# Kernel tuning notes

Measured on AMD Instinct MI355X. Metric: run time of the kernel, lower is better.

## Reference

```python
import jax, jax.numpy as jnp
import numpy as np

DELAY_TAPS = np.array([1, 4, 24, 96, 168])
MAX_DELAY = int(DELAY_TAPS.max())
LEAK_RATE = 0.1
RESERVOIR_DIM = 256
INPUT_DIM = 1
N_TAPS = len(DELAY_TAPS)
TARGET_RADIUS = 0.95


def setup_inputs() -> dict:
    key = jax.random.key(0)
    kx, kin, kfb, kb = jax.random.split(key, 4)
    B, T = 64, 2048
    x = jax.random.normal(kx, (B, T, INPUT_DIM), dtype=jnp.float32)
    # W_in ~ U(-0.5, 0.5)
    W_in = jax.random.uniform(kin, (RESERVOIR_DIM, INPUT_DIM), dtype=jnp.float32,
                              minval=-0.5, maxval=0.5)
    # W_fb: sparse gaussian rescaled to ~per-tap spectral radius
    per_tap_radius = TARGET_RADIUS / np.sqrt(N_TAPS)
    kfb1, kfb2 = jax.random.split(kfb)
    W = jax.random.normal(kfb1, (N_TAPS, RESERVOIR_DIM, RESERVOIR_DIM), dtype=jnp.float32)
    mask = jax.random.uniform(kfb2, W.shape) < 0.1
    W = W * mask
    # approx spectral radius of sparse gaussian ~ sqrt(R * density)
    approx_radius = np.sqrt(RESERVOIR_DIM * 0.1)
    W_fb = W * (per_tap_radius / approx_radius)
    tap_weights = jnp.ones((N_TAPS,), dtype=jnp.float32)
    bias = jax.random.uniform(kb, (RESERVOIR_DIM,), dtype=jnp.float32,
                              minval=-0.1, maxval=0.1)
    return {"x": x, "W_in": W_in, "W_fb": W_fb,
            "tap_weights": tap_weights, "bias": bias}


def reference(x, W_in, W_fb, tap_weights, bias):
    B, T, _ = x.shape
    R = W_in.shape[0]
    # static gather positions into rolling history buffer of length MAX_DELAY
    # history[:, -1] holds state at t-1  ->  state at t - tau lives at MAX_DELAY - tau
    pos = MAX_DELAY - DELAY_TAPS  # numpy, static

    drive = jnp.einsum('bti,ri->btr', x, W_in)  # (B,T,R)
    tap_w = jax.nn.softmax(tap_weights)

    h0 = jnp.zeros((B, R), x.dtype)
    hist0 = jnp.zeros((B, MAX_DELAY, R), x.dtype)

    def step(carry, d_t):
        h, hist = carry
        delayed = hist[:, pos, :]  # (B,K,R)
        fb = jnp.einsum('k,bkr,krs->bs', tap_w, delayed, W_fb)
        h_new = (1.0 - LEAK_RATE) * h + LEAK_RATE * jnp.tanh(d_t + fb + bias)
        hist = jnp.concatenate([hist[:, 1:], h_new[:, None, :]], axis=1)
        return (h_new, hist), h_new

    drive_t = jnp.swapaxes(drive, 0, 1)  # (T,B,R)
    _, states = jax.lax.scan(step, (h0, hist0), drive_t)
    return jnp.swapaxes(states, 0, 1)  # (B,T,R)
```

## Files before the change

### kernel.cpp

```cpp
#include <hip/hip_runtime.h>
#include <math.h>

typedef __attribute__((ext_vector_type(8))) short bf16x8;
typedef __attribute__((ext_vector_type(4))) float f32x4;

#define BB 64
#define TT 2048
#define RR 256
#define BLK 24
#define NTHR 512
#define HB_PAD 776
#define HW_PAD 264

#define MFMA(a, b, c) __builtin_amdgcn_mfma_f32_16x16x32_bf16((a), (b), (c), 0, 0, 0)

__device__ __forceinline__ unsigned short f2bf(float f) {
    unsigned u = __float_as_uint(f);
    return (unsigned short)((u + 0x7FFFu + ((u >> 16) & 1u)) >> 16);
}
__device__ __forceinline__ float bf2f(unsigned short h) {
    return __uint_as_float(((unsigned)h) << 16);
}
__device__ __forceinline__ float fast_tanh(float x) {
    float e = __expf(2.0f * x);
    return 1.0f - 2.0f * __builtin_amdgcn_rcpf(1.0f + e);
}

__global__ void pack_weights(const float* __restrict__ W_fb,
                             const float* __restrict__ tapw,
                             unsigned short* __restrict__ bp) {
    int gid = blockIdx.x * 256 + threadIdx.x;
    int l = gid & 63, c = gid >> 6;
    int tap = c >> 7;
    int rem = c & 127;
    int kt = rem >> 4, nt = rem & 15;

    float v0 = tapw[0], v1 = tapw[1], v2 = tapw[2], v3 = tapw[3], v4 = tapw[4];
    float mx = fmaxf(fmaxf(fmaxf(v0, v1), fmaxf(v2, v3)), v4);
    float e0 = expf(v0 - mx), e1 = expf(v1 - mx), e2 = expf(v2 - mx),
          e3 = expf(v3 - mx), e4 = expf(v4 - mx);
    float inv = 1.0f / (e0 + e1 + e2 + e3 + e4);
    float tws[5] = {e0 * inv, e1 * inv, e2 * inv, e3 * inv, e4 * inv};
    float tw = tws[tap];

    int kbase = 32 * kt + 8 * (l >> 4);
    int n = 16 * nt + (l & 15);
    const float* W = W_fb + tap * 65536;
    unsigned short t[8];
#pragma unroll
    for (int j = 0; j < 8; ++j) t[j] = f2bf(tw * W[(kbase + j) * 256 + n]);
    uint4 o;
    o.x = (unsigned)t[0] | ((unsigned)t[1] << 16);
    o.y = (unsigned)t[2] | ((unsigned)t[3] << 16);
    o.z = (unsigned)t[4] | ((unsigned)t[5] << 16);
    o.w = (unsigned)t[6] | ((unsigned)t[7] << 16);
    *(uint4*)(bp + (size_t)(c * 64 + l) * 8) = o;
}

__global__ __launch_bounds__(NTHR, 1)
void reservoir_mfma(const float* __restrict__ x,
                    const float* __restrict__ W_in,
                    const float* __restrict__ bias,
                    const unsigned short* __restrict__ bp,
                    float* __restrict__ out)
{
    const int b    = blockIdx.x;
    const int tid  = threadIdx.x;
    const int lane = tid & 63;
    const int w    = tid >> 6;
    const int l15  = lane & 15;
    const int quad = lane >> 4;

    __shared__ float xs[TT];
    __shared__ unsigned short hwinb[8][2][HW_PAD];
    __shared__ unsigned short hbcb[BLK][2][HB_PAD];
    __shared__ float Gl[BLK][257];
    __shared__ float hob[BLK][RR];

    for (int i = tid; i < TT; i += NTHR) xs[i] = x[b * TT + i];
    {
        unsigned* hz = (unsigned*)&hwinb[0][0][0];
        for (int i = tid; i < 8 * 2 * HW_PAD / 2; i += NTHR) hz[i] = 0u;
    }

    const bf16x8* bpv = (const bf16x8*)bp;
    bf16x8 b1[8][2], b4[8][2];
#pragma unroll
    for (int kt = 0; kt < 8; ++kt)
#pragma unroll
        for (int u = 0; u < 2; ++u) {
            int nt = 2 * w + u;
            b1[kt][u] = bpv[((0 * 8 + kt) * 16 + nt) * 64 + lane];
            b4[kt][u] = bpv[((1 * 8 + kt) * 16 + nt) * 64 + lane];
        }

    const int s0g = 32 * w + l15, s1g = s0g + 16;
    const float win0 = W_in[s0g], win1 = W_in[s1g];
    const float bi0 = bias[s0g], bi1 = bias[s1g];
    float hp0 = 0.0f, hp1 = 0.0f;

    const float* outr = out + (size_t)b * TT * RR;
    float*       outw = out + (size_t)b * TT * RR;

    const unsigned short* hw1v = &hwinb[0][l15 & 1][0];
    const unsigned short* hw4v = &hwinb[0][(l15 >> 2) & 1][0];
    const unsigned short* fa1 = &hbcb[16 + (l15 & 7)][(l15 >> 3) & 1][0];
    const size_t HWSLOT = 2 * HW_PAD;

    __syncthreads();

    for (int t0 = 0; t0 < TT; t0 += BLK) {
#pragma unroll
        for (int it = 0; it < 9; ++it) {
            int i = it * NTHR + tid;
            int j = i / 192;
            int p = i - j * 192;
            int r = 4 * p;
            int kf = r >> 8, rr = r & 255;
            float4 v = {0.f, 0.f, 0.f, 0.f};
            if (kf == 0) {
                if (t0 > 0) v = *(const float4*)&hob[j][rr];
            } else {
                int dk = (kf == 1) ? 96 : 168;
                int tt = t0 + j - dk;
                if (tt >= 0) v = *(const float4*)(outr + (size_t)tt * RR + rr);
            }
            unsigned short h0 = f2bf(v.x), h1 = f2bf(v.y), h2 = f2bf(v.z), h3 = f2bf(v.w);
            unsigned short q0 = f2bf(v.x - bf2f(h0)), q1 = f2bf(v.y - bf2f(h1)),
                           q2 = f2bf(v.z - bf2f(h2)), q3 = f2bf(v.w - bf2f(h3));
            uint2 H = { (unsigned)h0 | ((unsigned)h1 << 16), (unsigned)h2 | ((unsigned)h3 << 16) };
            uint2 Q = { (unsigned)q0 | ((unsigned)q1 << 16), (unsigned)q2 | ((unsigned)q3 << 16) };
            *(uint2*)&hbcb[j][0][r] = H;
            *(uint2*)&hbcb[j][1][r] = Q;
        }
        __syncthreads();

        f32x4 zf = {0.f, 0.f, 0.f, 0.f};
        f32x4 cf00a = zf, cf01a = zf, cf00b = zf, cf01b = zf, cf10 = zf, cf11 = zf;
        const int r0a = l15;
        bf16x8 nB0 = bpv[((16 + 0) * 16 + 2 * w + 0) * 64 + lane];
        bf16x8 nB1 = bpv[((16 + 0) * 16 + 2 * w + 1) * 64 + lane];
#pragma unroll 1
        for (int ft = 0; ft < 24; ++ft) {
            bf16x8 B0 = nB0, B1 = nB1;
            int nf = (ft < 23) ? ft + 1 : 23;
            nB0 = bpv[((16 + nf) * 16 + 2 * w + 0) * 64 + lane];
            nB1 = bpv[((16 + nf) * 16 + 2 * w + 1) * 64 + lane];
            int ro = 32 * ft + 8 * quad;
            bf16x8 a00 = *(const bf16x8*)&hbcb[r0a][0][ro];
            bf16x8 a01 = *(const bf16x8*)&hbcb[r0a][1][ro];
            bf16x8 a1  = *(const bf16x8*)&fa1[ro];
            cf00a = MFMA(a00, B0, cf00a); cf01a = MFMA(a00, B1, cf01a);
            cf00b = MFMA(a01, B0, cf00b); cf01b = MFMA(a01, B1, cf01b);
            cf10  = MFMA(a1,  B0, cf10);  cf11  = MFMA(a1,  B1, cf11);
        }
        f32x4 cf00 = cf00a + cf00b, cf01 = cf01a + cf01b;
        float cf10f[4], cf11f[4];
#pragma unroll
        for (int i = 0; i < 4; ++i) {
            cf10f[i] = cf10[i] + __shfl_xor(cf10[i], 32, 64);
            cf11f[i] = cf11[i] + __shfl_xor(cf11[i], 32, 64);
        }
#pragma unroll
        for (int i = 0; i < 4; ++i) {
            int j0 = 4 * quad + i;
            int tx0 = t0 + j0; float xv0 = xs[tx0 < TT ? tx0 : TT - 1];
            Gl[j0][s0g] = cf00[i] + bi0 + xv0 * win0;
            Gl[j0][s1g] = cf01[i] + bi1 + xv0 * win1;
            int j1 = 16 + 4 * quad + i;
            if (j1 < BLK) {
                int tx1 = t0 + j1; float xv1 = xs[tx1 < TT ? tx1 : TT - 1];
                Gl[j1][s0g] = cf10f[i] + bi0 + xv1 * win0;
                Gl[j1][s1g] = cf11f[i] + bi1 + xv1 * win1;
            }
        }
        __syncthreads();

        const int tend = (t0 + BLK < TT) ? (t0 + BLK) : TT;
#pragma unroll 1
        for (int t4 = t0; t4 < tend; t4 += 4) {
            f32x4 c40 = zf, c41 = zf;
            const int sl = (t4 - 4 + (l15 & 3)) & 7;
            const unsigned short* hw4 = hw4v + (size_t)sl * HWSLOT;
#pragma unroll
            for (int kt = 0; kt < 8; ++kt) {
                int ro = 32 * kt + 8 * quad;
                bf16x8 a = *(const bf16x8*)&hw4[ro];
                c40 = MFMA(a, b4[kt][0], c40);
                c41 = MFMA(a, b4[kt][1], c41);
            }
            float c40f[4], c41f[4];
#pragma unroll
            for (int u2 = 0; u2 < 4; ++u2) {
                c40f[u2] = c40[u2] + __shfl_xor(c40[u2], 16, 64);
                c41f[u2] = c41[u2] + __shfl_xor(c41[u2], 16, 64);
            }
#pragma unroll
            for (int u = 0; u < 4; ++u) {
                const int t = t4 + u;
                const int sp = (t - 1) & 7;
                const unsigned short* hw1 = hw1v + (size_t)sp * HWSLOT;
                f32x4 c10 = zf, c11 = zf;
#pragma unroll
                for (int kt = 0; kt < 8; ++kt) {
                    int ro = 32 * kt + 8 * quad;
                    bf16x8 a = *(const bf16x8*)&hw1[ro];
                    c10 = MFMA(a, b1[kt][0], c10);
                    c11 = MFMA(a, b1[kt][1], c11);
                }
                int jj = t - t0;
                float f0 = (c10[0] + c10[1]) + c40f[u] + Gl[jj][s0g];
                float f1 = (c11[0] + c11[1]) + c41f[u] + Gl[jj][s1g];
                float h0 = 0.9f * hp0 + 0.1f * fast_tanh(f0);
                float h1 = 0.9f * hp1 + 0.1f * fast_tanh(f1);
                hp0 = h0; hp1 = h1;
                const int wsl = t & 7;
                if (lane < 16) {
                    unsigned short hh0 = f2bf(h0), hh1 = f2bf(h1);
                    hwinb[wsl][0][s0g] = hh0;
                    hwinb[wsl][0][s1g] = hh1;
                    hwinb[wsl][1][s0g] = f2bf(h0 - bf2f(hh0));
                    hwinb[wsl][1][s1g] = f2bf(h1 - bf2f(hh1));
                    hob[jj][s0g] = h0;
                    hob[jj][s1g] = h1;
                }
                __syncthreads();
            }
        }

        {
            const int nf4 = (tend - t0) * (RR / 4);
            const float4* src = (const float4*)&hob[0][0];
            float4* dst = (float4*)(outw + (size_t)t0 * RR);
#pragma unroll
            for (int it = 0; it < 3; ++it) {
                int idx = it * NTHR + tid;
                if (idx < nf4) dst[idx] = src[idx];
            }
        }
    }
}

extern "C" void kernel_launch(void* const* d_in, const int* in_sizes, int n_in,
                              void* d_out, int out_size, void* d_ws, size_t ws_size,
                              hipStream_t stream) {
    const float* x    = (const float*)d_in[0];
    const float* W_in = (const float*)d_in[1];
    const float* W_fb = (const float*)d_in[2];
    const float* tapw = (const float*)d_in[3];
    const float* bias = (const float*)d_in[4];
    float* out = (float*)d_out;
    unsigned short* bp = (unsigned short*)d_ws;

    pack_weights<<<160, 256, 0, stream>>>(W_fb, tapw, bp);
    reservoir_mfma<<<BB, NTHR, 0, stream>>>(x, W_in, bias, bp, out);
}
```

Before: 2.214 ms.

## Halve block to 4 waves, each owning four 16-column output tiles

```diff
diff --git a/kernel.cpp b/kernel.cpp
--- a/kernel.cpp
+++ b/kernel.cpp
@@ -8,9 +8,9 @@
 #define TT 2048
 #define RR 256
 #define BLK 24
-#define NTHR 512
+#define NTHR 256
 #define HB_PAD 776
-#define HW_PAD 264
+#define HW_PAD 288
 
 #define MFMA(a, b, c) __builtin_amdgcn_mfma_f32_16x16x32_bf16((a), (b), (c), 0, 0, 0)
 
@@ -84,34 +84,38 @@
     }
 
     const bf16x8* bpv = (const bf16x8*)bp;
-    bf16x8 b1[8][2], b4[8][2];
+    bf16x8 b1[8][4], b4[8][4];
 #pragma unroll
     for (int kt = 0; kt < 8; ++kt)
 #pragma unroll
-        for (int u = 0; u < 2; ++u) {
-            int nt = 2 * w + u;
+        for (int u = 0; u < 4; ++u) {
+            int nt = 4 * w + u;
             b1[kt][u] = bpv[((0 * 8 + kt) * 16 + nt) * 64 + lane];
             b4[kt][u] = bpv[((1 * 8 + kt) * 16 + nt) * 64 + lane];
         }
 
-    const int s0g = 32 * w + l15, s1g = s0g + 16;
-    const float win0 = W_in[s0g], win1 = W_in[s1g];
-    const float bi0 = bias[s0g], bi1 = bias[s1g];
-    float hp0 = 0.0f, hp1 = 0.0f;
+    float win[4], bi[4], hp[4];
+#pragma unroll
+    for (int nt = 0; nt < 4; ++nt) {
+        int s = 64 * w + 16 * nt + l15;
+        win[nt] = W_in[s];
+        bi[nt]  = bias[s];
+        hp[nt]  = 0.0f;
+    }
 
     const float* outr = out + (size_t)b * TT * RR;
     float*       outw = out + (size_t)b * TT * RR;
 
     const unsigned short* hw1v = &hwinb[0][l15 & 1][0];
     const unsigned short* hw4v = &hwinb[0][(l15 >> 2) & 1][0];
-    const unsigned short* fa1 = &hbcb[16 + (l15 & 7)][(l15 >> 3) & 1][0];
+    const unsigned short* fa1  = &hbcb[16 + (l15 & 7)][(l15 >> 3) & 1][0];
     const size_t HWSLOT = 2 * HW_PAD;
 
     __syncthreads();
 
     for (int t0 = 0; t0 < TT; t0 += BLK) {
 #pragma unroll
-        for (int it = 0; it < 9; ++it) {
+        for (int it = 0; it < 18; ++it) {
             int i = it * NTHR + tid;
             int j = i / 192;
             int p = i - j * 192;
@@ -136,42 +140,57 @@
         __syncthreads();
 
         f32x4 zf = {0.f, 0.f, 0.f, 0.f};
-        f32x4 cf00a = zf, cf01a = zf, cf00b = zf, cf01b = zf, cf10 = zf, cf11 = zf;
+        f32x4 cf0a[4], cf0b[4], cf1[4];
+#pragma unroll
+        for (int nt = 0; nt < 4; ++nt) { cf0a[nt] = zf; cf0b[nt] = zf; cf1[nt] = zf; }
         const int r0a = l15;
-        bf16x8 nB0 = bpv[((16 + 0) * 16 + 2 * w + 0) * 64 + lane];
-        bf16x8 nB1 = bpv[((16 + 0) * 16 + 2 * w + 1) * 64 + lane];
+        bf16x8 nB[4];
+#pragma unroll
+        for (int nt = 0; nt < 4; ++nt)
+            nB[nt] = bpv[((16 + 0) * 16 + 4 * w + nt) * 64 + lane];
 #pragma unroll 1
         for (int ft = 0; ft < 24; ++ft) {
-            bf16x8 B0 = nB0, B1 = nB1;
+            bf16x8 B[4];
+#pragma unroll
+            for (int nt = 0; nt < 4; ++nt) B[nt] = nB[nt];
             int nf = (ft < 23) ? ft + 1 : 23;
-            nB0 = bpv[((16 + nf) * 16 + 2 * w + 0) * 64 + lane];
-            nB1 = bpv[((16 + nf) * 16 + 2 * w + 1) * 64 + lane];
+#pragma unroll
+            for (int nt = 0; nt < 4; ++nt)
+                nB[nt] = bpv[((16 + nf) * 16 + 4 * w + nt) * 64 + lane];
             int ro = 32 * ft + 8 * quad;
             bf16x8 a00 = *(const bf16x8*)&hbcb[r0a][0][ro];
             bf16x8 a01 = *(const bf16x8*)&hbcb[r0a][1][ro];
             bf16x8 a1  = *(const bf16x8*)&fa1[ro];
-            cf00a = MFMA(a00, B0, cf00a); cf01a = MFMA(a00, B1, cf01a);
-            cf00b = MFMA(a01, B0, cf00b); cf01b = MFMA(a01, B1, cf01b);
-            cf10  = MFMA(a1,  B0, cf10);  cf11  = MFMA(a1,  B1, cf11);
-        }
-        f32x4 cf00 = cf00a + cf00b, cf01 = cf01a + cf01b;
-        float cf10f[4], cf11f[4];
-#pragma unroll
-        for (int i = 0; i < 4; ++i) {
-            cf10f[i] = cf10[i] + __shfl_xor(cf10[i], 32, 64);
-            cf11f[i] = cf11[i] + __shfl_xor(cf11[i], 32, 64);
-        }
+#pragma unroll
+            for (int nt = 0; nt < 4; ++nt) {
+                cf0a[nt] = MFMA(a00, B[nt], cf0a[nt]);
+                cf0b[nt] = MFMA(a01, B[nt], cf0b[nt]);
+                cf1[nt]  = MFMA(a1,  B[nt], cf1[nt]);
+            }
+        }
+        float cf1f[4][4];
+#pragma unroll
+        for (int nt = 0; nt < 4; ++nt)
+#pragma unroll
+            for (int i = 0; i < 4; ++i)
+                cf1f[nt][i] = cf1[nt][i] + __shfl_xor(cf1[nt][i], 32, 64);
 #pragma unroll
         for (int i = 0; i < 4; ++i) {
             int j0 = 4 * quad + i;
             int tx0 = t0 + j0; float xv0 = xs[tx0 < TT ? tx0 : TT - 1];
-            Gl[j0][s0g] = cf00[i] + bi0 + xv0 * win0;
-            Gl[j0][s1g] = cf01[i] + bi1 + xv0 * win1;
+#pragma unroll
+            for (int nt = 0; nt < 4; ++nt) {
+                int s = 64 * w + 16 * nt + l15;
+                Gl[j0][s] = (cf0a[nt][i] + cf0b[nt][i]) + bi[nt] + xv0 * win[nt];
+            }
             int j1 = 16 + 4 * quad + i;
             if (j1 < BLK) {
                 int tx1 = t0 + j1; float xv1 = xs[tx1 < TT ? tx1 : TT - 1];
-                Gl[j1][s0g] = cf10f[i] + bi0 + xv1 * win0;
-                Gl[j1][s1g] = cf11f[i] + bi1 + xv1 * win1;
+#pragma unroll
+                for (int nt = 0; nt < 4; ++nt) {
+                    int s = 64 * w + 16 * nt + l15;
+                    Gl[j1][s] = cf1f[nt][i] + bi[nt] + xv1 * win[nt];
+                }
             }
         }
         __syncthreads();
@@ -179,50 +198,58 @@
         const int tend = (t0 + BLK < TT) ? (t0 + BLK) : TT;
 #pragma unroll 1
         for (int t4 = t0; t4 < tend; t4 += 4) {
-            f32x4 c40 = zf, c41 = zf;
+            f32x4 c4[4];
+#pragma unroll
+            for (int nt = 0; nt < 4; ++nt) c4[nt] = zf;
             const int sl = (t4 - 4 + (l15 & 3)) & 7;
             const unsigned short* hw4 = hw4v + (size_t)sl * HWSLOT;
 #pragma unroll
             for (int kt = 0; kt < 8; ++kt) {
                 int ro = 32 * kt + 8 * quad;
                 bf16x8 a = *(const bf16x8*)&hw4[ro];
-                c40 = MFMA(a, b4[kt][0], c40);
-                c41 = MFMA(a, b4[kt][1], c41);
-            }
-            float c40f[4], c41f[4];
-#pragma unroll
-            for (int u2 = 0; u2 < 4; ++u2) {
-                c40f[u2] = c40[u2] + __shfl_xor(c40[u2], 16, 64);
-                c41f[u2] = c41[u2] + __shfl_xor(c41[u2], 16, 64);
-            }
+#pragma unroll
+                for (int nt = 0; nt < 4; ++nt) c4[nt] = MFMA(a, b4[kt][nt], c4[nt]);
+            }
+            float c4f[4][4];
+#pragma unroll
+            for (int nt = 0; nt < 4; ++nt)
+#pragma unroll
+                for (int u2 = 0; u2 < 4; ++u2)
+                    c4f[nt][u2] = c4[nt][u2] + __shfl_xor(c4[nt][u2], 16, 64);
 #pragma unroll
             for (int u = 0; u < 4; ++u) {
                 const int t = t4 + u;
                 const int sp = (t - 1) & 7;
                 const unsigned short* hw1 = hw1v + (size_t)sp * HWSLOT;
-                f32x4 c10 = zf, c11 = zf;
+                f32x4 c1[4];
+#pragma unroll
+                for (int nt = 0; nt < 4; ++nt) c1[nt] = zf;
 #pragma unroll
                 for (int kt = 0; kt < 8; ++kt) {
                     int ro = 32 * kt + 8 * quad;
                     bf16x8 a = *(const bf16x8*)&hw1[ro];
-                    c10 = MFMA(a, b1[kt][0], c10);
-                    c11 = MFMA(a, b1[kt][1], c11);
-                }
-                int jj = t - t0;
-                float f0 = (c10[0] + c10[1]) + c40f[u] + Gl[jj][s0g];
-                float f1 = (c11[0] + c11[1]) + c41f[u] + Gl[jj][s1g];
-                float h0 = 0.9f * hp0 + 0.1f * fast_tanh(f0);
-                float h1 = 0.9f * hp1 + 0.1f * fast_tanh(f1);
-                hp0 = h0; hp1 = h1;
+#pragma unroll
+                    for (int nt = 0; nt < 4; ++nt) c1[nt] = MFMA(a, b1[kt][nt], c1[nt]);
+                }
+                const int jj = t - t0;
                 const int wsl = t & 7;
+                float hn[4];
+#pragma unroll
+                for (int nt = 0; nt < 4; ++nt) {
+                    int s = 64 * w + 16 * nt + l15;
+                    float f = (c1[nt][0] + c1[nt][1]) + c4f[nt][u] + Gl[jj][s];
+                    hn[nt] = 0.9f * hp[nt] + 0.1f * fast_tanh(f);
+                    hp[nt] = hn[nt];
+                }
                 if (lane < 16) {
-                    unsigned short hh0 = f2bf(h0), hh1 = f2bf(h1);
-                    hwinb[wsl][0][s0g] = hh0;
-                    hwinb[wsl][0][s1g] = hh1;
-                    hwinb[wsl][1][s0g] = f2bf(h0 - bf2f(hh0));
-                    hwinb[wsl][1][s1g] = f2bf(h1 - bf2f(hh1));
-                    hob[jj][s0g] = h0;
-                    hob[jj][s1g] = h1;
+#pragma unroll
+                    for (int nt = 0; nt < 4; ++nt) {
+                        int s = 64 * w + 16 * nt + l15;
+                        unsigned short hh = f2bf(hn[nt]);
+                        hwinb[wsl][0][s] = hh;
+                        hwinb[wsl][1][s] = f2bf(hn[nt] - bf2f(hh));
+                        hob[jj][s] = hn[nt];
+                    }
                 }
                 __syncthreads();
             }
@@ -233,7 +260,7 @@
             const float4* src = (const float4*)&hob[0][0];
             float4* dst = (float4*)(outw + (size_t)t0 * RR);
 #pragma unroll
-            for (int it = 0; it < 3; ++it) {
+            for (int it = 0; it < 6; ++it) {
                 int idx = it * NTHR + tid;
                 if (idx < nf4) dst[idx] = src[idx];
             }
```

Measured after the change: 2.990 ms. 35.1% more time.

## Spread per-step state writes across lanes, pack G as float2, deepen weight prefetch

Applied to the files above, without the earlier changes.

```diff
diff --git a/kernel.cpp b/kernel.cpp
--- a/kernel.cpp
+++ b/kernel.cpp
@@ -10,7 +10,7 @@
 #define BLK 24
 #define NTHR 512
 #define HB_PAD 776
-#define HW_PAD 264
+#define HW_PAD 288
 
 #define MFMA(a, b, c) __builtin_amdgcn_mfma_f32_16x16x32_bf16((a), (b), (c), 0, 0, 0)
 
@@ -74,7 +74,7 @@
     __shared__ float xs[TT];
     __shared__ unsigned short hwinb[8][2][HW_PAD];
     __shared__ unsigned short hbcb[BLK][2][HB_PAD];
-    __shared__ float Gl[BLK][257];
+    __shared__ float2 Gl2[BLK][130];
     __shared__ float hob[BLK][RR];
 
     for (int i = tid; i < TT; i += NTHR) xs[i] = x[b * TT + i];
@@ -104,8 +104,13 @@
 
     const unsigned short* hw1v = &hwinb[0][l15 & 1][0];
     const unsigned short* hw4v = &hwinb[0][(l15 >> 2) & 1][0];
-    const unsigned short* fa1 = &hbcb[16 + (l15 & 7)][(l15 >> 3) & 1][0];
+    const unsigned short* fa1  = &hbcb[16 + (l15 & 7)][(l15 >> 3) & 1][0];
     const size_t HWSLOT = 2 * HW_PAD;
+
+    const int varw  = quad >> 1;
+    const int s_w   = 32 * w + l15 + ((quad & 1) << 4);
+    unsigned short* const hwb = &hwinb[0][0][0];
+    const unsigned hw_off = (unsigned)(varw * HW_PAD + s_w);
 
     __syncthreads();
 
@@ -138,21 +143,52 @@
         f32x4 zf = {0.f, 0.f, 0.f, 0.f};
         f32x4 cf00a = zf, cf01a = zf, cf00b = zf, cf01b = zf, cf10 = zf, cf11 = zf;
         const int r0a = l15;
-        bf16x8 nB0 = bpv[((16 + 0) * 16 + 2 * w + 0) * 64 + lane];
-        bf16x8 nB1 = bpv[((16 + 0) * 16 + 2 * w + 1) * 64 + lane];
+        const int cw0 = 2 * w, cw1 = 2 * w + 1;
+        bf16x8 p0A = bpv[((16 + 0) * 16 + cw0) * 64 + lane];
+        bf16x8 p0B = bpv[((16 + 0) * 16 + cw1) * 64 + lane];
+        bf16x8 p1A = bpv[((16 + 1) * 16 + cw0) * 64 + lane];
+        bf16x8 p1B = bpv[((16 + 1) * 16 + cw1) * 64 + lane];
+        bf16x8 p2A = bpv[((16 + 2) * 16 + cw0) * 64 + lane];
+        bf16x8 p2B = bpv[((16 + 2) * 16 + cw1) * 64 + lane];
 #pragma unroll 1
-        for (int ft = 0; ft < 24; ++ft) {
-            bf16x8 B0 = nB0, B1 = nB1;
-            int nf = (ft < 23) ? ft + 1 : 23;
-            nB0 = bpv[((16 + nf) * 16 + 2 * w + 0) * 64 + lane];
-            nB1 = bpv[((16 + nf) * 16 + 2 * w + 1) * 64 + lane];
-            int ro = 32 * ft + 8 * quad;
-            bf16x8 a00 = *(const bf16x8*)&hbcb[r0a][0][ro];
-            bf16x8 a01 = *(const bf16x8*)&hbcb[r0a][1][ro];
-            bf16x8 a1  = *(const bf16x8*)&fa1[ro];
-            cf00a = MFMA(a00, B0, cf00a); cf01a = MFMA(a00, B1, cf01a);
-            cf00b = MFMA(a01, B0, cf00b); cf01b = MFMA(a01, B1, cf01b);
-            cf10  = MFMA(a1,  B0, cf10);  cf11  = MFMA(a1,  B1, cf11);
+        for (int g = 0; g < 8; ++g) {
+            const int base = 3 * g;
+            {
+                int ro = 32 * base + 8 * quad;
+                bf16x8 a00 = *(const bf16x8*)&hbcb[r0a][0][ro];
+                bf16x8 a01 = *(const bf16x8*)&hbcb[r0a][1][ro];
+                bf16x8 a1  = *(const bf16x8*)&fa1[ro];
+                cf00a = MFMA(a00, p0A, cf00a); cf01a = MFMA(a00, p0B, cf01a);
+                cf00b = MFMA(a01, p0A, cf00b); cf01b = MFMA(a01, p0B, cf01b);
+                cf10  = MFMA(a1,  p0A, cf10);  cf11  = MFMA(a1,  p0B, cf11);
+                int nf = base + 3; if (nf > 23) nf = 23;
+                p0A = bpv[((16 + nf) * 16 + cw0) * 64 + lane];
+                p0B = bpv[((16 + nf) * 16 + cw1) * 64 + lane];
+            }
+            {
+                int ro = 32 * (base + 1) + 8 * quad;
+                bf16x8 a00 = *(const bf16x8*)&hbcb[r0a][0][ro];
+                bf16x8 a01 = *(const bf16x8*)&hbcb[r0a][1][ro];
+                bf16x8 a1  = *(const bf16x8*)&fa1[ro];
+                cf00a = MFMA(a00, p1A, cf00a); cf01a = MFMA(a00, p1B, cf01a);
+                cf00b = MFMA(a01, p1A, cf00b); cf01b = MFMA(a01, p1B, cf01b);
+                cf10  = MFMA(a1,  p1A, cf10);  cf11  = MFMA(a1,  p1B, cf11);
+                int nf = base + 4; if (nf > 23) nf = 23;
+                p1A = bpv[((16 + nf) * 16 + cw0) * 64 + lane];
+                p1B = bpv[((16 + nf) * 16 + cw1) * 64 + lane];
+            }
+            {
+                int ro = 32 * (base + 2) + 8 * quad;
+                bf16x8 a00 = *(const bf16x8*)&hbcb[r0a][0][ro];
+                bf16x8 a01 = *(const bf16x8*)&hbcb[r0a][1][ro];
+                bf16x8 a1  = *(const bf16x8*)&fa1[ro];
+                cf00a = MFMA(a00, p2A, cf00a); cf01a = MFMA(a00, p2B, cf01a);
+                cf00b = MFMA(a01, p2A, cf00b); cf01b = MFMA(a01, p2B, cf01b);
+                cf10  = MFMA(a1,  p2A, cf10);  cf11  = MFMA(a1,  p2B, cf11);
+                int nf = base + 5; if (nf > 23) nf = 23;
+                p2A = bpv[((16 + nf) * 16 + cw0) * 64 + lane];
+                p2B = bpv[((16 + nf) * 16 + cw1) * 64 + lane];
+            }
         }
         f32x4 cf00 = cf00a + cf00b, cf01 = cf01a + cf01b;
         float cf10f[4], cf11f[4];
@@ -165,13 +201,13 @@
         for (int i = 0; i < 4; ++i) {
             int j0 = 4 * quad + i;
             int tx0 = t0 + j0; float xv0 = xs[tx0 < TT ? tx0 : TT - 1];
-            Gl[j0][s0g] = cf00[i] + bi0 + xv0 * win0;
-            Gl[j0][s1g] = cf01[i] + bi1 + xv0 * win1;
+            Gl2[j0][16 * w + l15] =
+                make_float2(cf00[i] + bi0 + xv0 * win0, cf01[i] + bi1 + xv0 * win1);
             int j1 = 16 + 4 * quad + i;
             if (j1 < BLK) {
                 int tx1 = t0 + j1; float xv1 = xs[tx1 < TT ? tx1 : TT - 1];
-                Gl[j1][s0g] = cf10f[i] + bi0 + xv1 * win0;
-                Gl[j1][s1g] = cf11f[i] + bi1 + xv1 * win1;
+                Gl2[j1][16 * w + l15] =
+                    make_float2(cf10f[i] + bi0 + xv1 * win0, cf11f[i] + bi1 + xv1 * win1);
             }
         }
         __syncthreads();
@@ -208,22 +244,21 @@
                     c10 = MFMA(a, b1[kt][0], c10);
                     c11 = MFMA(a, b1[kt][1], c11);
                 }
-                int jj = t - t0;
-                float f0 = (c10[0] + c10[1]) + c40f[u] + Gl[jj][s0g];
-                float f1 = (c11[0] + c11[1]) + c41f[u] + Gl[jj][s1g];
+                const int jj = t - t0;
+                const int wsl = t & 7;
+                float2 gl = Gl2[jj][16 * w + l15];
+                float f0 = (c10[0] + c10[1]) + c40f[u] + gl.x;
+                float f1 = (c11[0] + c11[1]) + c41f[u] + gl.y;
                 float h0 = 0.9f * hp0 + 0.1f * fast_tanh(f0);
                 float h1 = 0.9f * hp1 + 0.1f * fast_tanh(f1);
                 hp0 = h0; hp1 = h1;
-                const int wsl = t & 7;
-                if (lane < 16) {
-                    unsigned short hh0 = f2bf(h0), hh1 = f2bf(h1);
-                    hwinb[wsl][0][s0g] = hh0;
-                    hwinb[wsl][0][s1g] = hh1;
-                    hwinb[wsl][1][s0g] = f2bf(h0 - bf2f(hh0));
-                    hwinb[wsl][1][s1g] = f2bf(h1 - bf2f(hh1));
-                    hob[jj][s0g] = h0;
-                    hob[jj][s1g] = h1;
-                }
+                unsigned short hh0 = f2bf(h0), hh1 = f2bf(h1);
+                unsigned short lo0 = f2bf(h0 - bf2f(hh0)), lo1 = f2bf(h1 - bf2f(hh1));
+                unsigned short v0 = varw ? lo0 : hh0;
+                unsigned short v1 = varw ? lo1 : hh1;
+                unsigned short wv = (quad & 1) ? v1 : v0;
+                hwb[(size_t)wsl * HWSLOT + hw_off] = wv;
+                if (quad < 2) hob[jj][s_w] = (quad & 1) ? h1 : h0;
                 __syncthreads();
             }
         }
```

After: 1.960 ms. -11.5%, faster.
